# Kernel optimization log

Measured on AMD Instinct MI355X. Metric: run time of the kernel, lower is better.

The kernel has to match this reference:

```python
import jax, jax.numpy as jnp
import numpy as np

D_MODEL, N_HEAD, D_HEAD = 1024, 16, 64
B, QLEN, MLEN = 4, 1024, 1024
KLEN = QLEN + MLEN  # == rlen
NEG_INF = -1e30


def _rel_shift(x):
    # x: [b, q, rlen, n] -> Transformer-XL relative shift along axis 2
    b, q, rl, n = x.shape
    zero_pad = jnp.zeros((b, q, 1, n), dtype=x.dtype)
    x_padded = jnp.concatenate([zero_pad, x], axis=2)          # [b, q, rl+1, n]
    x_padded = x_padded.reshape(b, rl + 1, q, n)
    return x_padded[:, 1:].reshape(b, q, rl, n)


def setup_inputs() -> dict:
    key = jax.random.key(0)
    ks = jax.random.split(key, 8)
    s = 1.0 / np.sqrt(D_MODEL)
    w = jax.random.normal(ks[0], (B, KLEN, D_MODEL), jnp.float32)
    r = jax.random.normal(ks[1], (1, KLEN, D_MODEL), jnp.float32)
    Wq = jax.random.normal(ks[2], (D_MODEL, N_HEAD * D_HEAD), jnp.float32) * s
    Wkv = jax.random.normal(ks[3], (D_MODEL, 2 * N_HEAD * D_HEAD), jnp.float32) * s
    Wr = jax.random.normal(ks[4], (D_MODEL, N_HEAD * D_HEAD), jnp.float32) * s
    Wo = jax.random.normal(ks[5], (N_HEAD * D_HEAD, D_MODEL), jnp.float32) * s
    bias_w = jax.random.normal(ks[6], (N_HEAD, D_HEAD), jnp.float32) * 0.02
    bias_r = jax.random.normal(ks[7], (N_HEAD, D_HEAD), jnp.float32) * 0.02
    # causal-with-memory mask: query i attends to keys j <= i + MLEN
    i = jnp.arange(QLEN)[:, None]
    j = jnp.arange(KLEN)[None, :]
    attn_mask = j > (i + MLEN)  # True => masked
    return {"w": w, "r": r, "Wq": Wq, "Wkv": Wkv, "Wr": Wr, "Wo": Wo,
            "bias_w": bias_w, "bias_r": bias_r, "attn_mask": attn_mask,
            "qlen": QLEN}


def reference(w, r, Wq, Wkv, Wr, Wo, bias_w, bias_r, attn_mask, qlen):
    bsz, klen, _ = w.shape
    rlen = r.shape[1]
    scale = 1.0 / np.sqrt(D_HEAD)

    q = (w[:, -qlen:] @ Wq).reshape(bsz, qlen, N_HEAD, D_HEAD)
    kv = w @ Wkv
    k, v = jnp.split(kv, 2, axis=-1)
    k = k.reshape(bsz, klen, N_HEAD, D_HEAD)
    v = v.reshape(bsz, klen, N_HEAD, D_HEAD)
    rk = (r @ Wr).reshape(rlen, N_HEAD, D_HEAD)

    AC = jnp.einsum('bind,bjnd->bijn', q + bias_w, k)
    BD = jnp.einsum('bind,jnd->bijn', q + bias_r, rk)
    score = (AC + _rel_shift(BD)) * scale
    score = jnp.where(attn_mask[None, :, :, None], NEG_INF, score)
    prob = jax.nn.softmax(score, axis=2)
    attn_vec = jnp.einsum('bijn,bjnd->bind', prob, v)
    attn_vec = attn_vec.reshape(bsz, qlen, N_HEAD * D_HEAD)
    return attn_vec @ Wo
```

## Files before the change

### kernel.cpp

```cpp
#include <hip/hip_runtime.h>
#include <hip/hip_bf16.h>
#include <stdint.h>


#define DEVI static __device__ __forceinline__

typedef __attribute__((ext_vector_type(8))) short  s8v;
typedef __attribute__((ext_vector_type(4))) float  f4v;
typedef __attribute__((ext_vector_type(2))) int    i2v;
typedef __attribute__((ext_vector_type(4))) float  fl4;

DEVI unsigned short f2b(float f) {
  __hip_bfloat16 h = __float2bfloat16(f);
  return __builtin_bit_cast(unsigned short, h);
}

DEVI f4v MFMA(s8v a, s8v b, f4v c) {
  return __builtin_amdgcn_mfma_f32_16x16x32_bf16(a, b, c, 0, 0, 0);
}

DEVI void gl_lds16(const void* g, void* lds) {
  __builtin_amdgcn_global_load_lds(
      (const __attribute__((address_space(1))) unsigned int*)g,
      (__attribute__((address_space(3))) unsigned int*)lds, 16, 0, 0);
}

__global__ void transpose_bf(const float* __restrict__ W,
                             unsigned short* __restrict__ WT, int N) {
  __shared__ float tile[32][33];
  int n0 = blockIdx.x * 32, k0 = blockIdx.y * 32;
  int tx = threadIdx.x, ty = threadIdx.y;
#pragma unroll
  for (int i = 0; i < 4; ++i)
    tile[ty + i * 8][tx] = W[(size_t)(k0 + ty + i * 8) * N + n0 + tx];
  __syncthreads();
#pragma unroll
  for (int i = 0; i < 4; ++i)
    WT[(size_t)(n0 + ty + i * 8) * 1024 + k0 + tx] = f2b(tile[tx][ty + i * 8]);
}

__global__ void transpose_v(const unsigned short* __restrict__ in,
                            unsigned short* __restrict__ out) {
  __shared__ unsigned short Ts[64 * 72];
  const int t = threadIdx.x;
  const int j0 = blockIdx.x * 64;
  const size_t bh = blockIdx.y;
#pragma unroll
  for (int p = 0; p < 2; ++p) {
    int cc = t + p * 256;
    int j = cc >> 3, d0 = (cc & 7) * 8;
    s8v v = *(const s8v*)(in + (bh * 2048 + j0 + j) * 64 + d0);
    *(s8v*)(Ts + j * 72 + d0) = v;
  }
  __syncthreads();
  const int d = t >> 2, jc = (t & 3) * 16;
  s8v a, b;
#pragma unroll
  for (int e = 0; e < 8; ++e) a[e] = (short)Ts[(jc + e) * 72 + d];
#pragma unroll
  for (int e = 0; e < 8; ++e) b[e] = (short)Ts[(jc + 8 + e) * 72 + d];
  *(s8v*)(out + (bh * 64 + d) * 2048 + j0 + jc) = a;
  *(s8v*)(out + (bh * 64 + d) * 2048 + j0 + jc + 8) = b;
}

template <int MODE>
__global__ __launch_bounds__(256, 2) void gemm_kern(
    const float* __restrict__ A, const unsigned short* __restrict__ A16,
    const unsigned short* __restrict__ BT, unsigned short* __restrict__ O1,
    unsigned short* __restrict__ O2, float* __restrict__ Of,
    const float* __restrict__ biasw, const float* __restrict__ biasr) {
  __shared__ unsigned short As[128 * 32];
  __shared__ unsigned short Bs[128 * 32];
  const int t = threadIdx.x, l = t & 63, w = t >> 6;
  const int g = l >> 4, lr = l & 15;
  const int bm = blockIdx.x, bn = blockIdx.y;
  const int wr = w >> 1, wc = w & 1;
  f4v acc[4][4] = {};

  for (int k0 = 0; k0 < 1024; k0 += 32) {
#pragma unroll
    for (int ss = 0; ss < 2; ++ss) {
      int idx = w * 64 + ss * 256 + l;
      int row = idx >> 2, c = idx & 3;
      gl_lds16(BT + (size_t)(bn * 128 + row) * 1024 + k0 + c * 8,
               (void*)(Bs + (size_t)(w * 64 + ss * 256) * 8));
    }
    if (MODE == 3) {
#pragma unroll
      for (int ss = 0; ss < 2; ++ss) {
        int idx = w * 64 + ss * 256 + l;
        int row = idx >> 2, c = idx & 3;
        gl_lds16(A16 + (size_t)(bm * 128 + row) * 1024 + k0 + c * 8,
                 (void*)(As + (size_t)(w * 64 + ss * 256) * 8));
      }
    } else {
#pragma unroll
      for (int ss = 0; ss < 4; ++ss) {
        int idx = t + ss * 256;
        int row = idx >> 3, c = idx & 7;
        int grow = bm * 128 + row;
        size_t arow = (MODE == 0)
                          ? ((size_t)(grow >> 10) * 2048 + 1024 + (grow & 1023))
                          : (size_t)grow;
        fl4 v = *(const fl4*)(A + arow * 1024 + k0 + c * 4);
        unsigned int p0 = f2b(v.x) | ((unsigned int)f2b(v.y) << 16);
        unsigned int p1 = f2b(v.z) | ((unsigned int)f2b(v.w) << 16);
        i2v pv; pv.x = (int)p0; pv.y = (int)p1;
        *(i2v*)(As + row * 32 + c * 4) = pv;
      }
    }
    __syncthreads();

    s8v af[4], bf[4];
#pragma unroll
    for (int m = 0; m < 4; ++m)
      af[m] = *(const s8v*)(As + (wr * 64 + m * 16 + lr) * 32 + g * 8);
#pragma unroll
    for (int n = 0; n < 4; ++n)
      bf[n] = *(const s8v*)(Bs + (wc * 64 + n * 16 + lr) * 32 + g * 8);
#pragma unroll
    for (int m = 0; m < 4; ++m)
#pragma unroll
      for (int n = 0; n < 4; ++n) acc[m][n] = MFMA(af[m], bf[n], acc[m][n]);
    __syncthreads();
  }

#pragma unroll
  for (int m = 0; m < 4; ++m) {
#pragma unroll
    for (int n = 0; n < 4; ++n) {
#pragma unroll
      for (int r = 0; r < 4; ++r) {
        int row = bm * 128 + wr * 64 + m * 16 + g * 4 + r;
        int col = bn * 128 + wc * 64 + n * 16 + lr;
        float v = acc[m][n][r];
        if (MODE == 0) {
          int b = row >> 10, i = row & 1023;
          int nh = col >> 6, d = col & 63;
          size_t o = ((size_t)(b * 16 + nh) * 1024 + i) * 64 + d;
          O1[o] = f2b(v + biasw[col]);
          O2[o] = f2b(v + biasr[col]);
        } else if (MODE == 1) {
          int b = row >> 11, j = row & 2047;
          if (col < 1024)
            O1[((size_t)(b * 16 + (col >> 6)) * 2048 + j) * 64 + (col & 63)] =
                f2b(v);
          else
            O2[((size_t)(b * 16 + ((col - 1024) >> 6)) * 2048 + j) * 64 +
               (col & 63)] = f2b(v);
        } else if (MODE == 2) {
          O1[((size_t)(col >> 6) * 2048 + row) * 64 + (col & 63)] = f2b(v);
        } else {
          Of[(size_t)row * 1024 + col] = v;
        }
      }
    }
  }
}

__global__ __launch_bounds__(256, 2) void attn_kern(
    const unsigned short* __restrict__ qw, const unsigned short* __restrict__ qr,
    const unsigned short* __restrict__ kk, const unsigned short* __restrict__ vt,
    const unsigned short* __restrict__ rkp, unsigned short* __restrict__ av) {
  __shared__ unsigned short Ks[64 * 64];
  __shared__ unsigned short Vs[64 * 64];
  __shared__ unsigned short Rs[128 * 64];
  __shared__ unsigned short Pn[4][1024];
  const int t = threadIdx.x, l = t & 63, w = t >> 6;
  const int g = l >> 4, lr = l & 15;
  const int i0 = blockIdx.x * 64, n = blockIdx.y, b = blockIdx.z;
  const size_t bn = (size_t)(b * 16 + n);
  const unsigned short* qwb = qw + bn * 1024 * 64;
  const unsigned short* qrb = qr + bn * 1024 * 64;
  const unsigned short* kb = kk + bn * 2048 * 64;
  const unsigned short* vb = vt + bn * 64 * 2048;
  const unsigned short* rb = rkp + (size_t)n * 2048 * 64;

  const int qi = i0 + w * 16 + lr;
  s8v aqw[2], aqr[2];
#pragma unroll
  for (int ks = 0; ks < 2; ++ks) {
    aqw[ks] = *(const s8v*)(qwb + (size_t)qi * 64 + ks * 32 + g * 8);
    aqr[ks] = *(const s8v*)(qrb + (size_t)qi * 64 + ks * 32 + g * 8);
  }

  f4v acco[4] = {};
  float mrow[4] = {-3e38f, -3e38f, -3e38f, -3e38f};
  float lrow[4] = {};

  const float SC = 0.18033688f;

  const int ntile = (i0 + 1088) >> 6;
  for (int jt = 0; jt < ntile; ++jt) {
    const int j0 = jt * 64;
    const int m0 = j0 + 960 - i0;
#pragma unroll
    for (int ss = 0; ss < 2; ++ss) {
      int idx = w * 64 + ss * 256 + l;
      int row = idx >> 3, c = idx & 7;
      gl_lds16(kb + (size_t)(j0 + row) * 64 + ((c ^ (row & 7)) * 8),
               (void*)(Ks + (size_t)(w * 64 + ss * 256) * 8));
    }
#pragma unroll
    for (int ss = 0; ss < 2; ++ss) {
      int idx = w * 64 + ss * 256 + l;
      int d = idx >> 3, c = idx & 7;
      gl_lds16(vb + (size_t)d * 2048 + j0 + ((c ^ (d & 7)) * 8),
               (void*)(Vs + (size_t)(w * 64 + ss * 256) * 8));
    }
#pragma unroll
    for (int ss = 0; ss < 4; ++ss) {
      int idx = w * 64 + ss * 256 + l;
      int rr = idx >> 3, c = idx & 7;
      int m = m0 + rr;
      if (m > 2047) m = 2047;
      gl_lds16(rb + (size_t)m * 64 + ((c ^ (rr & 7)) * 8),
               (void*)(Rs + (size_t)(w * 64 + ss * 256) * 8));
    }
    __syncthreads();

    f4v accs[4] = {};
    f4v acce[5] = {};
#pragma unroll
    for (int ks = 0; ks < 2; ++ks) {
#pragma unroll
      for (int jf = 0; jf < 4; ++jf) {
        int row = jf * 16 + lr;
        s8v bk = *(const s8v*)(Ks + row * 64 + (((ks * 4 + g) ^ (row & 7)) * 8));
        accs[jf] = MFMA(aqw[ks], bk, accs[jf]);
      }
#pragma unroll
      for (int ef = 0; ef < 5; ++ef) {
        int row = (3 - w + ef) * 16 + lr;
        s8v br = *(const s8v*)(Rs + row * 64 + (((ks * 4 + g) ^ (row & 7)) * 8));
        acce[ef] = MFMA(aqr[ks], br, acce[ef]);
      }
    }

    float P[4][4];
    float corr[4];
#pragma unroll
    for (int r = 0; r < 4; ++r) {
      const int s = 15 - 4 * g - r;
      const int src = (l & 48) | ((lr + s) & 15);
      const int carry = (lr + s) >> 4;
      float rmax = -3e38f;
#pragma unroll
      for (int jf = 0; jf < 4; ++jf) {
        float e0 = __shfl(acce[jf][r], src, 64);
        float e1 = __shfl(acce[jf + 1][r], src, 64);
        float ev = carry ? e1 : e0;
        float sv = (accs[jf][r] + ev) * SC;
        int jg = j0 + jf * 16 + lr;
        int ig = i0 + w * 16 + 4 * g + r;
        if (jg > ig + 1024) sv = -3e38f;
        P[jf][r] = sv;
        rmax = fmaxf(rmax, sv);
      }
#pragma unroll
      for (int dd = 1; dd < 16; dd <<= 1)
        rmax = fmaxf(rmax, __shfl_xor(rmax, dd, 64));
      float nm = fmaxf(mrow[r], rmax);
      corr[r] = exp2f(mrow[r] - nm);
      mrow[r] = nm;
      float psum = 0.f;
#pragma unroll
      for (int jf = 0; jf < 4; ++jf) {
        float p = exp2f(P[jf][r] - nm);
        P[jf][r] = p;
        psum += p;
      }
#pragma unroll
      for (int dd = 1; dd < 16; dd <<= 1) psum += __shfl_xor(psum, dd, 64);
      lrow[r] = lrow[r] * corr[r] + psum;
    }
#pragma unroll
    for (int df = 0; df < 4; ++df)
#pragma unroll
      for (int r = 0; r < 4; ++r) acco[df][r] *= corr[r];

#pragma unroll
    for (int jf = 0; jf < 4; ++jf) {
#pragma unroll
      for (int r = 0; r < 4; ++r) {
        int ip = 4 * g + r;
        int cj = (jf * 2 + (lr >> 3)) ^ (ip & 7);
        Pn[w][ip * 64 + cj * 8 + (lr & 7)] = f2b(P[jf][r]);
      }
    }
    asm volatile("s_waitcnt lgkmcnt(0)" ::: "memory");
    __builtin_amdgcn_sched_barrier(0);

#pragma unroll
    for (int ks = 0; ks < 2; ++ks) {
      s8v ap = *(const s8v*)(Pn[w] + lr * 64 + (((ks * 4 + g) ^ (lr & 7)) * 8));
#pragma unroll
      for (int df = 0; df < 4; ++df) {
        int vrow = df * 16 + lr;
        s8v bv =
            *(const s8v*)(Vs + vrow * 64 + (((ks * 4 + g) ^ (vrow & 7)) * 8));
        acco[df] = MFMA(ap, bv, acco[df]);
      }
    }
    __syncthreads();
  }

#pragma unroll
  for (int r = 0; r < 4; ++r) {
    float inv = 1.0f / lrow[r];
    int ig = i0 + w * 16 + 4 * g + r;
#pragma unroll
    for (int df = 0; df < 4; ++df)
      av[((size_t)b * 1024 + ig) * 1024 + n * 64 + df * 16 + lr] =
          f2b(acco[df][r] * inv);
  }
}

extern "C" void kernel_launch(void* const* d_in, const int* in_sizes, int n_in,
                              void* d_out, int out_size, void* d_ws,
                              size_t ws_size, hipStream_t stream) {
  (void)in_sizes; (void)n_in; (void)out_size; (void)ws_size;
  const float* w   = (const float*)d_in[0];
  const float* r   = (const float*)d_in[1];
  const float* Wq  = (const float*)d_in[2];
  const float* Wkv = (const float*)d_in[3];
  const float* Wr  = (const float*)d_in[4];
  const float* Wo  = (const float*)d_in[5];
  const float* bw  = (const float*)d_in[6];
  const float* br  = (const float*)d_in[7];

  char* ws = (char*)d_ws;
  const size_t MB = 1024 * 1024;
  unsigned short* WqT  = (unsigned short*)(ws + 0 * MB);
  unsigned short* WkvT = (unsigned short*)(ws + 2 * MB);
  unsigned short* WrT  = (unsigned short*)(ws + 6 * MB);
  unsigned short* WoT  = (unsigned short*)(ws + 8 * MB);
  unsigned short* qwb  = (unsigned short*)(ws + 10 * MB);
  unsigned short* qrb  = (unsigned short*)(ws + 18 * MB);
  unsigned short* kbf  = (unsigned short*)(ws + 26 * MB);
  unsigned short* vbf  = (unsigned short*)(ws + 42 * MB);
  unsigned short* rkb  = (unsigned short*)(ws + 58 * MB);
  unsigned short* avb  = (unsigned short*)(ws + 62 * MB);
  unsigned short* vtb  = (unsigned short*)d_out;

  dim3 tb(32, 8);
  hipLaunchKernelGGL(transpose_bf, dim3(32, 32), tb, 0, stream, Wq, WqT, 1024);
  hipLaunchKernelGGL(transpose_bf, dim3(64, 32), tb, 0, stream, Wkv, WkvT, 2048);
  hipLaunchKernelGGL(transpose_bf, dim3(32, 32), tb, 0, stream, Wr, WrT, 1024);
  hipLaunchKernelGGL(transpose_bf, dim3(32, 32), tb, 0, stream, Wo, WoT, 1024);

  hipLaunchKernelGGL((gemm_kern<0>), dim3(32, 8), dim3(256), 0, stream,
                     w, (const unsigned short*)nullptr, WqT, qwb, qrb,
                     (float*)nullptr, bw, br);
  hipLaunchKernelGGL((gemm_kern<1>), dim3(64, 16), dim3(256), 0, stream,
                     w, (const unsigned short*)nullptr, WkvT, kbf, vbf,
                     (float*)nullptr, (const float*)nullptr,
                     (const float*)nullptr);
  hipLaunchKernelGGL((gemm_kern<2>), dim3(16, 8), dim3(256), 0, stream,
                     r, (const unsigned short*)nullptr, WrT, rkb,
                     (unsigned short*)nullptr, (float*)nullptr,
                     (const float*)nullptr, (const float*)nullptr);

  hipLaunchKernelGGL(transpose_v, dim3(32, 64), dim3(256), 0, stream, vbf, vtb);

  hipLaunchKernelGGL(attn_kern, dim3(16, 16, 4), dim3(256), 0, stream,
                     qwb, qrb, kbf, vtb, rkb, avb);

  hipLaunchKernelGGL((gemm_kern<3>), dim3(32, 8), dim3(256), 0, stream,
                     (const float*)nullptr, avb, WoT, (unsigned short*)nullptr,
                     (unsigned short*)nullptr, (float*)d_out,
                     (const float*)nullptr, (const float*)nullptr);
}
```

Before: 455.2 us.

## Double-buffer LDS tiles in GEMM and attention, merge weight transposes

Adds two LDS buffers to the GEMM and attention kernels so the global-to-LDS loads for the next K or key tile are issued before computing on the current tile, with one barrier per iteration instead of two. The fp32 A operand in the GEMM is prefetched into registers and converted and written after the MFMAs. The attention causal mask check now runs only on the last key tile. The four weight transpose launches are merged into one. LDS use per block doubles, which could lower occupancy, especially in the attention kernel, and it also raises register pressure.

```diff
diff --git a/kernel.cpp b/kernel.cpp
--- a/kernel.cpp
+++ b/kernel.cpp
@@ -25,10 +25,24 @@
       (__attribute__((address_space(3))) unsigned int*)lds, 16, 0, 0);
 }
 
-__global__ void transpose_bf(const float* __restrict__ W,
-                             unsigned short* __restrict__ WT, int N) {
+__global__ void transpose_all(const float* __restrict__ Wq,
+                              const float* __restrict__ Wkv,
+                              const float* __restrict__ Wr,
+                              const float* __restrict__ Wo,
+                              unsigned short* __restrict__ WqT,
+                              unsigned short* __restrict__ WkvT,
+                              unsigned short* __restrict__ WrT,
+                              unsigned short* __restrict__ WoT) {
   __shared__ float tile[32][33];
-  int n0 = blockIdx.x * 32, k0 = blockIdx.y * 32;
+  const int bx = blockIdx.x;
+  const float* W;
+  unsigned short* WT;
+  int N, nb;
+  if (bx < 32)       { W = Wq;  WT = WqT;  N = 1024; nb = bx; }
+  else if (bx < 96)  { W = Wkv; WT = WkvT; N = 2048; nb = bx - 32; }
+  else if (bx < 128) { W = Wr;  WT = WrT;  N = 1024; nb = bx - 96; }
+  else               { W = Wo;  WT = WoT;  N = 1024; nb = bx - 128; }
+  int n0 = nb * 32, k0 = blockIdx.y * 32;
   int tx = threadIdx.x, ty = threadIdx.y;
 #pragma unroll
   for (int i = 0; i < 4; ++i)
@@ -69,60 +83,91 @@
     const unsigned short* __restrict__ BT, unsigned short* __restrict__ O1,
     unsigned short* __restrict__ O2, float* __restrict__ Of,
     const float* __restrict__ biasw, const float* __restrict__ biasr) {
-  __shared__ unsigned short As[128 * 32];
-  __shared__ unsigned short Bs[128 * 32];
+  __shared__ unsigned short As[2][128 * 32];
+  __shared__ unsigned short Bs[2][128 * 32];
   const int t = threadIdx.x, l = t & 63, w = t >> 6;
   const int g = l >> 4, lr = l & 15;
   const int bm = blockIdx.x, bn = blockIdx.y;
   const int wr = w >> 1, wc = w & 1;
   f4v acc[4][4] = {};
 
-  for (int k0 = 0; k0 < 1024; k0 += 32) {
+  auto stageB = [&](int k0, int buf) {
 #pragma unroll
     for (int ss = 0; ss < 2; ++ss) {
       int idx = w * 64 + ss * 256 + l;
       int row = idx >> 2, c = idx & 3;
       gl_lds16(BT + (size_t)(bn * 128 + row) * 1024 + k0 + c * 8,
-               (void*)(Bs + (size_t)(w * 64 + ss * 256) * 8));
-    }
-    if (MODE == 3) {
-#pragma unroll
-      for (int ss = 0; ss < 2; ++ss) {
-        int idx = w * 64 + ss * 256 + l;
-        int row = idx >> 2, c = idx & 3;
-        gl_lds16(A16 + (size_t)(bm * 128 + row) * 1024 + k0 + c * 8,
-                 (void*)(As + (size_t)(w * 64 + ss * 256) * 8));
-      }
-    } else {
-#pragma unroll
-      for (int ss = 0; ss < 4; ++ss) {
-        int idx = t + ss * 256;
-        int row = idx >> 3, c = idx & 7;
-        int grow = bm * 128 + row;
-        size_t arow = (MODE == 0)
-                          ? ((size_t)(grow >> 10) * 2048 + 1024 + (grow & 1023))
-                          : (size_t)grow;
-        fl4 v = *(const fl4*)(A + arow * 1024 + k0 + c * 4);
-        unsigned int p0 = f2b(v.x) | ((unsigned int)f2b(v.y) << 16);
-        unsigned int p1 = f2b(v.z) | ((unsigned int)f2b(v.w) << 16);
-        i2v pv; pv.x = (int)p0; pv.y = (int)p1;
-        *(i2v*)(As + row * 32 + c * 4) = pv;
-      }
-    }
+               (void*)(Bs[buf] + (w * 64 + ss * 256) * 8));
+    }
+  };
+  auto stageA_lds = [&](int k0, int buf) {
+#pragma unroll
+    for (int ss = 0; ss < 2; ++ss) {
+      int idx = w * 64 + ss * 256 + l;
+      int row = idx >> 2, c = idx & 3;
+      gl_lds16(A16 + (size_t)(bm * 128 + row) * 1024 + k0 + c * 8,
+               (void*)(As[buf] + (w * 64 + ss * 256) * 8));
+    }
+  };
+  auto loadA = [&](int k0, fl4* regs) {
+#pragma unroll
+    for (int ss = 0; ss < 4; ++ss) {
+      int idx = t + ss * 256;
+      int row = idx >> 3, c = idx & 7;
+      int grow = bm * 128 + row;
+      size_t arow = (MODE == 0)
+                        ? ((size_t)(grow >> 10) * 2048 + 1024 + (grow & 1023))
+                        : (size_t)grow;
+      regs[ss] = *(const fl4*)(A + arow * 1024 + k0 + c * 4);
+    }
+  };
+  auto writeA = [&](const fl4* regs, int buf) {
+#pragma unroll
+    for (int ss = 0; ss < 4; ++ss) {
+      int idx = t + ss * 256;
+      int row = idx >> 3, c = idx & 7;
+      fl4 v = regs[ss];
+      unsigned int p0 = f2b(v.x) | ((unsigned int)f2b(v.y) << 16);
+      unsigned int p1 = f2b(v.z) | ((unsigned int)f2b(v.w) << 16);
+      i2v pv; pv.x = (int)p0; pv.y = (int)p1;
+      *(i2v*)(As[buf] + row * 32 + c * 4) = pv;
+    }
+  };
+
+  stageB(0, 0);
+  if (MODE == 3) {
+    stageA_lds(0, 0);
+  } else {
+    fl4 r0[4];
+    loadA(0, r0);
+    writeA(r0, 0);
+  }
+  __syncthreads();
+
+  int cur = 0;
+  for (int step = 0; step < 32; ++step) {
+    const bool nx = step < 31;
+    const int nk0 = (step + 1) * 32;
+    fl4 aregs[4];
+    if (nx) {
+      stageB(nk0, cur ^ 1);
+      if (MODE == 3) stageA_lds(nk0, cur ^ 1);
+      else loadA(nk0, aregs);
+    }
+    s8v af[4], bf[4];
+#pragma unroll
+    for (int m = 0; m < 4; ++m)
+      af[m] = *(const s8v*)(As[cur] + (wr * 64 + m * 16 + lr) * 32 + g * 8);
+#pragma unroll
+    for (int n = 0; n < 4; ++n)
+      bf[n] = *(const s8v*)(Bs[cur] + (wc * 64 + n * 16 + lr) * 32 + g * 8);
+#pragma unroll
+    for (int m = 0; m < 4; ++m)
+#pragma unroll
+      for (int n = 0; n < 4; ++n) acc[m][n] = MFMA(af[m], bf[n], acc[m][n]);
+    if (nx && MODE != 3) writeA(aregs, cur ^ 1);
     __syncthreads();
-
-    s8v af[4], bf[4];
-#pragma unroll
-    for (int m = 0; m < 4; ++m)
-      af[m] = *(const s8v*)(As + (wr * 64 + m * 16 + lr) * 32 + g * 8);
-#pragma unroll
-    for (int n = 0; n < 4; ++n)
-      bf[n] = *(const s8v*)(Bs + (wc * 64 + n * 16 + lr) * 32 + g * 8);
-#pragma unroll
-    for (int m = 0; m < 4; ++m)
-#pragma unroll
-      for (int n = 0; n < 4; ++n) acc[m][n] = MFMA(af[m], bf[n], acc[m][n]);
-    __syncthreads();
+    cur ^= 1;
   }
 
 #pragma unroll
@@ -162,9 +207,9 @@
     const unsigned short* __restrict__ qw, const unsigned short* __restrict__ qr,
     const unsigned short* __restrict__ kk, const unsigned short* __restrict__ vt,
     const unsigned short* __restrict__ rkp, unsigned short* __restrict__ av) {
-  __shared__ unsigned short Ks[64 * 64];
-  __shared__ unsigned short Vs[64 * 64];
-  __shared__ unsigned short Rs[128 * 64];
+  __shared__ unsigned short Ks[2][64 * 64];
+  __shared__ unsigned short Vs[2][64 * 64];
+  __shared__ unsigned short Rs[2][128 * 64];
   __shared__ unsigned short Pn[4][1024];
   const int t = threadIdx.x, l = t & 63, w = t >> 6;
   const int g = l >> 4, lr = l & 15;
@@ -189,9 +234,9 @@
   float lrow[4] = {};
 
   const float SC = 0.18033688f;
-
   const int ntile = (i0 + 1088) >> 6;
-  for (int jt = 0; jt < ntile; ++jt) {
+
+  auto stage = [&](int jt, int buf) {
     const int j0 = jt * 64;
     const int m0 = j0 + 960 - i0;
 #pragma unroll
@@ -199,14 +244,14 @@
       int idx = w * 64 + ss * 256 + l;
       int row = idx >> 3, c = idx & 7;
       gl_lds16(kb + (size_t)(j0 + row) * 64 + ((c ^ (row & 7)) * 8),
-               (void*)(Ks + (size_t)(w * 64 + ss * 256) * 8));
+               (void*)(Ks[buf] + (w * 64 + ss * 256) * 8));
     }
 #pragma unroll
     for (int ss = 0; ss < 2; ++ss) {
       int idx = w * 64 + ss * 256 + l;
       int d = idx >> 3, c = idx & 7;
       gl_lds16(vb + (size_t)d * 2048 + j0 + ((c ^ (d & 7)) * 8),
-               (void*)(Vs + (size_t)(w * 64 + ss * 256) * 8));
+               (void*)(Vs[buf] + (w * 64 + ss * 256) * 8));
     }
 #pragma unroll
     for (int ss = 0; ss < 4; ++ss) {
@@ -215,9 +260,18 @@
       int m = m0 + rr;
       if (m > 2047) m = 2047;
       gl_lds16(rb + (size_t)m * 64 + ((c ^ (rr & 7)) * 8),
-               (void*)(Rs + (size_t)(w * 64 + ss * 256) * 8));
-    }
-    __syncthreads();
+               (void*)(Rs[buf] + (w * 64 + ss * 256) * 8));
+    }
+  };
+
+  stage(0, 0);
+  __syncthreads();
+
+  int cur = 0;
+  for (int jt = 0; jt < ntile; ++jt) {
+    const int j0 = jt * 64;
+    if (jt + 1 < ntile) stage(jt + 1, cur ^ 1);
+    const bool mt = (jt == ntile - 1);
 
     f4v accs[4] = {};
     f4v acce[5] = {};
@@ -226,13 +280,15 @@
 #pragma unroll
       for (int jf = 0; jf < 4; ++jf) {
         int row = jf * 16 + lr;
-        s8v bk = *(const s8v*)(Ks + row * 64 + (((ks * 4 + g) ^ (row & 7)) * 8));
+        s8v bk =
+            *(const s8v*)(Ks[cur] + row * 64 + (((ks * 4 + g) ^ (row & 7)) * 8));
         accs[jf] = MFMA(aqw[ks], bk, accs[jf]);
       }
 #pragma unroll
       for (int ef = 0; ef < 5; ++ef) {
         int row = (3 - w + ef) * 16 + lr;
-        s8v br = *(const s8v*)(Rs + row * 64 + (((ks * 4 + g) ^ (row & 7)) * 8));
+        s8v br =
+            *(const s8v*)(Rs[cur] + row * 64 + (((ks * 4 + g) ^ (row & 7)) * 8));
         acce[ef] = MFMA(aqr[ks], br, acce[ef]);
       }
     }
@@ -251,9 +307,11 @@
         float e1 = __shfl(acce[jf + 1][r], src, 64);
         float ev = carry ? e1 : e0;
         float sv = (accs[jf][r] + ev) * SC;
-        int jg = j0 + jf * 16 + lr;
-        int ig = i0 + w * 16 + 4 * g + r;
-        if (jg > ig + 1024) sv = -3e38f;
+        if (mt) {
+          int jg = j0 + jf * 16 + lr;
+          int ig = i0 + w * 16 + 4 * g + r;
+          if (jg > ig + 1024) sv = -3e38f;
+        }
         P[jf][r] = sv;
         rmax = fmaxf(rmax, sv);
       }
@@ -293,16 +351,18 @@
 
 #pragma unroll
     for (int ks = 0; ks < 2; ++ks) {
-      s8v ap = *(const s8v*)(Pn[w] + lr * 64 + (((ks * 4 + g) ^ (lr & 7)) * 8));
+      s8v ap =
+          *(const s8v*)(Pn[w] + lr * 64 + (((ks * 4 + g) ^ (lr & 7)) * 8));
 #pragma unroll
       for (int df = 0; df < 4; ++df) {
         int vrow = df * 16 + lr;
-        s8v bv =
-            *(const s8v*)(Vs + vrow * 64 + (((ks * 4 + g) ^ (vrow & 7)) * 8));
+        s8v bv = *(const s8v*)(Vs[cur] + vrow * 64 +
+                               (((ks * 4 + g) ^ (vrow & 7)) * 8));
         acco[df] = MFMA(ap, bv, acco[df]);
       }
     }
     __syncthreads();
+    cur ^= 1;
   }
 
 #pragma unroll
@@ -343,11 +403,8 @@
   unsigned short* avb  = (unsigned short*)(ws + 62 * MB);
   unsigned short* vtb  = (unsigned short*)d_out;
 
-  dim3 tb(32, 8);
-  hipLaunchKernelGGL(transpose_bf, dim3(32, 32), tb, 0, stream, Wq, WqT, 1024);
-  hipLaunchKernelGGL(transpose_bf, dim3(64, 32), tb, 0, stream, Wkv, WkvT, 2048);
-  hipLaunchKernelGGL(transpose_bf, dim3(32, 32), tb, 0, stream, Wr, WrT, 1024);
-  hipLaunchKernelGGL(transpose_bf, dim3(32, 32), tb, 0, stream, Wo, WoT, 1024);
+  hipLaunchKernelGGL(transpose_all, dim3(160, 32), dim3(32, 8), 0, stream,
+                     Wq, Wkv, Wr, Wo, WqT, WkvT, WrT, WoT);
 
   hipLaunchKernelGGL((gemm_kern<0>), dim3(32, 8), dim3(256), 0, stream,
                      w, (const unsigned short*)nullptr, WqT, qwb, qrb,
```

Measured after the change: 469.9 us. 1.03x slower.
